# Kernel optimization log

Hardware: AMD Instinct MI355X
Metric: run time of the kernel (lower is better)

The kernel has to match this reference:

```python
import jax, jax.numpy as jnp
import numpy as np

B, K, D = 32768, 64, 64
GAIN = 1.0
LOG_2PI = float(np.log(2.0 * np.pi))


def setup_inputs() -> dict:
    key = jax.random.key(0)
    k1, k2, k3, k4 = jax.random.split(key, 4)
    return {
        "x": jax.random.normal(k1, (B, D), jnp.float32),
        "means_raw": jax.random.normal(k2, (K, D), jnp.float32),
        "scale_raw": jax.random.normal(k3, (K, D, D), jnp.float32),
        "weights_raw": jax.random.normal(k4, (K,), jnp.float32),
    }


def reference(x, means_raw, scale_raw, weights_raw):
    # EqualizedLR reparametrization: w_eff = w * gain / sqrt(fan_in)
    means = means_raw * (GAIN / np.sqrt(K * D))              # [K, D]
    pre = scale_raw * (GAIN / np.sqrt(K * D * D))            # [K, D, D]
    # ExpScaleTril (diag=False): strict lower triangle + exp(diagonal)
    dvec = jnp.exp(jnp.diagonal(pre, axis1=-2, axis2=-1))    # [K, D]
    L = jnp.tril(pre, -1) + dvec[..., :, None] * jnp.eye(D, dtype=pre.dtype)  # [K, D, D]
    # mixture logits -> log weights (EqualizedLR then softmax parametrization)
    logw = jax.nn.log_softmax(weights_raw * (GAIN / np.sqrt(K)), axis=-1)    # [K]

    # Precompute L^{-1} per component (K,D small), then whiten via one big GEMM.
    eye = jnp.broadcast_to(jnp.eye(D, dtype=L.dtype), L.shape)
    Linv = jax.scipy.linalg.solve_triangular(L, eye, lower=True)             # [K, D, D]

    diff = x[:, None, :] - means[None, :, :]                 # [B, K, D]
    z = jnp.einsum('kij,bkj->bki', Linv, diff)               # whitened residuals [B, K, D]
    maha = jnp.sum(z * z, axis=-1)                           # [B, K]
    half_log_det = jnp.sum(jnp.log(dvec), axis=-1)           # [K]
    comp_lp = -0.5 * (maha + D * LOG_2PI) - half_log_det     # [B, K]

    lp = jax.scipy.special.logsumexp(comp_lp + logw, axis=-1)  # [B]
    return -jnp.mean(lp)
```

## Files before the change

kernel.cpp:

```cpp
#include <hip/hip_runtime.h>

#define LOG_2PI 1.8378770664093453f

typedef __attribute__((ext_vector_type(8))) short  short8;
typedef __attribute__((ext_vector_type(4))) float  float4_;

__device__ __forceinline__ unsigned short f2bf(float f) {
  unsigned u = __builtin_bit_cast(unsigned, f);
  u += 0x7fffu + ((u >> 16) & 1u);
  return (unsigned short)(u >> 16);
}
__device__ __forceinline__ float bf2f(unsigned short h) {
  unsigned u = ((unsigned)h) << 16;
  return __builtin_bit_cast(float, u);
}
template <int CTRL>
__device__ __forceinline__ float dpp_add(float v) {
  int t = __builtin_amdgcn_mov_dpp(__builtin_bit_cast(int, v), CTRL, 0xf, 0xf, true);
  return v + __builtin_bit_cast(float, t);
}
__device__ __forceinline__ void async16(const void* g, void* l) {
  __builtin_amdgcn_global_load_lds((const __attribute__((address_space(1))) unsigned int*)g,
                                   (__attribute__((address_space(3))) unsigned int*)l, 16, 0, 0);
}

__global__ __launch_bounds__(256) void gmm_setup(
    const float* __restrict__ means_raw, const float* __restrict__ scale_raw,
    const float* __restrict__ weights_raw, unsigned short* __restrict__ Wf)
{
  const int k = blockIdx.x;
  const int t = threadIdx.x;
  const int lane = t & 63;
  const int wv = t >> 6;
  const int q = lane >> 4;
  const int jj = lane & 15;

  __shared__ float Plt[64][68];
  __shared__ float Vt[64][68];
  __shared__ __align__(16) unsigned short Vb[64][72];
  __shared__ float dg[64], rdg[64], mu_s[64], y_s[64];

  {
    const int i = t >> 2;
    const int c0 = (t & 3) * 16;
    float4_ v4[4];
    const float4_* src = (const float4_*)(scale_raw + (size_t)k * 4096 + i * 64 + c0);
    v4[0] = src[0]; v4[1] = src[1]; v4[2] = src[2]; v4[3] = src[3];
#pragma unroll
    for (int e = 0; e < 16; ++e) {
      const int c = c0 + e;
      const float val = ((const float*)v4)[e] * (1.0f / 512.0f);
      Plt[c][i] = (c < i) ? val : 0.0f;
      if (c == i) { dg[i] = val; rdg[i] = __expf(-val); }
    }
  }
  if (t < 64) mu_s[t] = means_raw[k * 64 + t] * (1.0f / 64.0f);
  __syncthreads();

  {
    const int j = wv * 16 + jj;
    float s[16];
#pragma unroll
    for (int i = 0; i < 16; ++i) s[i] = 0.0f;
#pragma unroll
    for (int m = 0; m < 64; ++m) {
      const float rm = rdg[m];
      float vcand = (m == j) ? rm : -s[m & 15] * rm;
      const float v = __shfl(vcand, (m >> 4) * 16 + jj, 64);
      if (q == (m >> 4)) {
        Vt[j][m] = v;
        Vb[j][m] = f2bf(v);
      }
      const float4_* prow = (const float4_*)&Plt[m][16 * q];
      const float4_ p0 = prow[0], p1 = prow[1], p2 = prow[2], p3 = prow[3];
      s[0]  += p0[0] * v; s[1]  += p0[1] * v; s[2]  += p0[2] * v; s[3]  += p0[3] * v;
      s[4]  += p1[0] * v; s[5]  += p1[1] * v; s[6]  += p1[2] * v; s[7]  += p1[3] * v;
      s[8]  += p2[0] * v; s[9]  += p2[1] * v; s[10] += p2[2] * v; s[11] += p2[3] * v;
      s[12] += p3[0] * v; s[13] += p3[1] * v; s[14] += p3[2] * v; s[15] += p3[3] * v;
    }
  }
  __syncthreads();

  {
    unsigned short* Wk = Wf + (size_t)k * 4608;
    const short8 a0 = *(const short8*)&Vb[16 * wv + jj][8 * q];
    const short8 a1 = *(const short8*)&Vb[16 * wv + jj][8 * q + 32];
#pragma unroll
    for (int t4 = 0; t4 < 4; ++t4) {
      const short8 b0 = *(const short8*)&Vb[jj + 16 * t4][8 * q];
      const short8 b1 = *(const short8*)&Vb[jj + 16 * t4][8 * q + 32];
      float4_ f = {0.f, 0.f, 0.f, 0.f};
      f = __builtin_amdgcn_mfma_f32_16x16x32_bf16(a0, b0, f, 0, 0, 0);
      f = __builtin_amdgcn_mfma_f32_16x16x32_bf16(a1, b1, f, 0, 0, 0);
#pragma unroll
      for (int r = 0; r < 4; ++r)
        Wk[(16 * wv + 4 * q + r) * 72 + jj + 16 * t4] = f2bf(-0.5f * f[r]);
    }
  }
  if (wv == 0) {
    float acc = 0.0f;
    for (int j2 = 0; j2 < 64; ++j2) acc += Vt[j2][lane] * mu_s[j2];
    y_s[lane] = acc;
  }
  __syncthreads();

  if (t < 64) {
    const int i = t;
    float ci = 0.0f;
#pragma unroll
    for (int m4 = 0; m4 < 16; ++m4) {
      const float4_ a4 = *(const float4_*)&Vt[i][4 * m4];
      const float4_ b4 = *(const float4_*)&y_s[4 * m4];
      ci += a4[0] * b4[0] + a4[1] * b4[1] + a4[2] * b4[2] + a4[3] * b4[3];
    }
    char* Wk = (char*)(Wf + (size_t)k * 4608);
    *(float*)(Wk + i * 144 + 128) = ci;
    float rq  = ci * mu_s[i];
    float dgv = dg[i];
    const float wr = weights_raw[i] * 0.125f;
    float mx = wr;
#pragma unroll
    for (int d = 1; d < 64; d <<= 1) mx = fmaxf(mx, __shfl_xor(mx, d, 64));
    float se = __expf(wr - mx);
#pragma unroll
    for (int d = 1; d < 64; d <<= 1) {
      se  += __shfl_xor(se, d, 64);
      rq  += __shfl_xor(rq, d, 64);
      dgv += __shfl_xor(dgv, d, 64);
    }
    if (i == 0) {
      const float wrk  = weights_raw[k] * 0.125f;
      const float logw = wrk - mx - __logf(se);
      *(float*)(Wk + 132) = -0.5f * rq - 32.0f * LOG_2PI - dgv + logw;
    }
  }
}

__global__ __launch_bounds__(256, 4) void gmm_main(
    const float* __restrict__ x, const unsigned short* __restrict__ Wf,
    unsigned short* __restrict__ ph)
{
  __shared__ __align__(16) unsigned short Wlds[2][2][4608];

  const int t = threadIdx.x;
  const int lane = t & 63;
  const int wv = t >> 6;
  const int q = lane >> 4;
  const int lr = lane & 15;
  const int kh = blockIdx.x & 3;
  const int rt = blockIdx.x >> 2;
  const int rowBase = rt * 128 + wv * 32;
  const int kbase = kh * 16;

  short8 a[2][2];
#pragma unroll
  for (int mt = 0; mt < 2; ++mt)
#pragma unroll
    for (int ks = 0; ks < 2; ++ks) {
      const float4_* xv = (const float4_*)(x + (size_t)(rowBase + mt * 16 + lr) * 64 + ks * 32 + q * 8);
      const float4_ lo = xv[0], hi = xv[1];
      short8 v;
      v[0] = f2bf(lo[0]); v[1] = f2bf(lo[1]); v[2] = f2bf(lo[2]); v[3] = f2bf(lo[3]);
      v[4] = f2bf(hi[0]); v[5] = f2bf(hi[1]); v[6] = f2bf(hi[2]); v[7] = f2bf(hi[3]);
      a[mt][ks] = v;
    }

  float xc[2][4][4];
#pragma unroll
  for (int mt = 0; mt < 2; ++mt)
#pragma unroll
    for (int r = 0; r < 4; ++r) {
      const float* xp = x + (size_t)(rowBase + mt * 16 + q * 4 + r) * 64 + lr;
#pragma unroll
      for (int t4 = 0; t4 < 4; ++t4) xc[mt][t4][r] = xp[16 * t4];
    }

  float sacc[2][4] = {{0, 0, 0, 0}, {0, 0, 0, 0}};

#define STAGE(g, slot)                                                          \
  {                                                                             \
    const unsigned short* src = Wf + (size_t)(kbase + 2 * (g)) * 4608 + t * 8;  \
    unsigned short* dst = &Wlds[slot][0][0] + t * 8;                            \
    async16(src,         dst);                                                  \
    async16(src + 2048,  dst + 2048);                                           \
    async16(src + 4096,  dst + 4096);                                           \
    async16(src + 6144,  dst + 6144);                                           \
    if (t < 128) async16(src + 8192, dst + 8192);                               \
  }

  STAGE(0, 0)
  __syncthreads();

  for (int g = 0; g < 8; ++g) {
    const int cur = g & 1;
    if (g < 7) STAGE(g + 1, cur ^ 1)
#pragma unroll
    for (int kk = 0; kk < 2; ++kk) {
      const unsigned short* wb = &Wlds[cur][kk][0];
      float cc[4];
#pragma unroll
      for (int t4 = 0; t4 < 4; ++t4)
        cc[t4] = *(const float*)(wb + (lr + 16 * t4) * 72 + 64);
      const float bk = *(const float*)(wb + 66) + 90.0f;

      short8 b[2][4];
#pragma unroll
      for (int t4 = 0; t4 < 4; ++t4)
#pragma unroll
        for (int ks = 0; ks < 2; ++ks)
          b[ks][t4] = *(const short8*)(wb + (lr + 16 * t4) * 72 + 8 * q + 32 * ks);

      float4_ f[2][4];
#pragma unroll
      for (int mt = 0; mt < 2; ++mt)
#pragma unroll
        for (int t4 = 0; t4 < 4; ++t4) {
          const float cv = cc[t4];
          float4_ acc = {cv, cv, cv, cv};
          acc = __builtin_amdgcn_mfma_f32_16x16x32_bf16(a[mt][0], b[0][t4], acc, 0, 0, 0);
          acc = __builtin_amdgcn_mfma_f32_16x16x32_bf16(a[mt][1], b[1][t4], acc, 0, 0, 0);
          f[mt][t4] = acc;
        }

#pragma unroll
      for (int mt = 0; mt < 2; ++mt)
#pragma unroll
        for (int r = 0; r < 4; ++r) {
          float sdot = xc[mt][0][r] * f[mt][0][r] + xc[mt][1][r] * f[mt][1][r]
                     + xc[mt][2][r] * f[mt][2][r] + xc[mt][3][r] * f[mt][3][r];
          sdot = dpp_add<0x121>(sdot);
          sdot = dpp_add<0x122>(sdot);
          sdot = dpp_add<0x124>(sdot);
          sdot = dpp_add<0x128>(sdot);
          sacc[mt][r] += __expf(sdot + bk);
        }
    }
    __syncthreads();
  }
#undef STAGE

  if (lr == 0) {
#pragma unroll
    for (int mt = 0; mt < 2; ++mt)
#pragma unroll
      for (int r = 0; r < 4; ++r)
        ph[(size_t)kh * 32768 + rowBase + mt * 16 + q * 4 + r] = f2bf(sacc[mt][r]);
  }
}

__global__ __launch_bounds__(256) void gmm_final1(const unsigned short* __restrict__ ph,
                                                  float* __restrict__ p1)
{
  const int t = threadIdx.x;
  const int r0 = blockIdx.x * 512 + t;
  float v = 0.0f;
#pragma unroll
  for (int h = 0; h < 2; ++h) {
    const int row = r0 + 256 * h;
    const float s = bf2f(ph[row]) + bf2f(ph[32768 + row])
                  + bf2f(ph[65536 + row]) + bf2f(ph[98304 + row]);
    v += __logf(s) - 90.0f;
  }
#pragma unroll
  for (int d = 1; d < 64; d <<= 1) v += __shfl_xor(v, d, 64);
  __shared__ float s4[4];
  if ((t & 63) == 0) s4[t >> 6] = v;
  __syncthreads();
  if (t == 0) p1[blockIdx.x] = s4[0] + s4[1] + s4[2] + s4[3];
}

__global__ __launch_bounds__(64) void gmm_final2(const float* __restrict__ p1,
                                                 float* __restrict__ out)
{
  float v = p1[threadIdx.x];
#pragma unroll
  for (int d = 1; d < 64; d <<= 1) v += __shfl_xor(v, d, 64);
  if (threadIdx.x == 0) out[0] = -v * (1.0f / 32768.0f);
}

extern "C" void kernel_launch(void* const* d_in, const int* in_sizes, int n_in,
                              void* d_out, int out_size, void* d_ws, size_t ws_size,
                              hipStream_t stream)
{
  const float* x           = (const float*)d_in[0];
  const float* means_raw   = (const float*)d_in[1];
  const float* scale_raw   = (const float*)d_in[2];
  const float* weights_raw = (const float*)d_in[3];
  float* out = (float*)d_out;

  char* ws = (char*)d_ws;
  unsigned short* Wf = (unsigned short*)ws;
  unsigned short* ph = (unsigned short*)(ws + 589824);
  float* p1          = (float*)(ws + 851968);

  gmm_setup<<<64, 256, 0, stream>>>(means_raw, scale_raw, weights_raw, Wf);
  gmm_main<<<1024, 256, 0, stream>>>(x, Wf, ph);
  gmm_final1<<<64, 256, 0, stream>>>(ph, p1);
  gmm_final2<<<1, 64, 0, stream>>>(p1, out);
}
```

Before: 109.4 us.

## Fuse final reductions into main kernel via atomics and last-block finish

Removes the two final reduction kernels. The main kernel now atomically adds per-row partial sums into an fp32 buffer, and the last block to finish (tracked by an atomic counter) computes the log-mean itself. The grid is doubled, so each block handles 8 components instead of 16, which raises parallelism. The log2e scaling is folded into the setup weights so the inner loop can use exp2. The changes trade two launches for atomic traffic and a serial tail reduction run by a single block.

```diff
diff --git a/kernel.cpp b/kernel.cpp
--- a/kernel.cpp
+++ b/kernel.cpp
@@ -1,6 +1,7 @@
 #include <hip/hip_runtime.h>
 
 #define LOG_2PI 1.8378770664093453f
+#define LOG2E   1.4426950408889634f
 
 typedef __attribute__((ext_vector_type(8))) short  short8;
 typedef __attribute__((ext_vector_type(4))) float  float4_;
@@ -10,10 +11,6 @@
   u += 0x7fffu + ((u >> 16) & 1u);
   return (unsigned short)(u >> 16);
 }
-__device__ __forceinline__ float bf2f(unsigned short h) {
-  unsigned u = ((unsigned)h) << 16;
-  return __builtin_bit_cast(float, u);
-}
 template <int CTRL>
 __device__ __forceinline__ float dpp_add(float v) {
   int t = __builtin_amdgcn_mov_dpp(__builtin_bit_cast(int, v), CTRL, 0xf, 0xf, true);
@@ -26,7 +23,8 @@
 
 __global__ __launch_bounds__(256) void gmm_setup(
     const float* __restrict__ means_raw, const float* __restrict__ scale_raw,
-    const float* __restrict__ weights_raw, unsigned short* __restrict__ Wf)
+    const float* __restrict__ weights_raw, unsigned short* __restrict__ Wf,
+    float* __restrict__ ph, unsigned int* __restrict__ done)
 {
   const int k = blockIdx.x;
   const int t = threadIdx.x;
@@ -34,6 +32,10 @@
   const int wv = t >> 6;
   const int q = lane >> 4;
   const int jj = lane & 15;
+
+  ph[k * 512 + t] = 0.0f;
+  ph[k * 512 + 256 + t] = 0.0f;
+  if (k == 0 && t == 0) *done = 0u;
 
   __shared__ float Plt[64][68];
   __shared__ float Vt[64][68];
@@ -94,7 +96,7 @@
       f = __builtin_amdgcn_mfma_f32_16x16x32_bf16(a1, b1, f, 0, 0, 0);
 #pragma unroll
       for (int r = 0; r < 4; ++r)
-        Wk[(16 * wv + 4 * q + r) * 72 + jj + 16 * t4] = f2bf(-0.5f * f[r]);
+        Wk[(16 * wv + 4 * q + r) * 72 + jj + 16 * t4] = f2bf(-0.5f * LOG2E * f[r]);
     }
   }
   if (wv == 0) {
@@ -114,7 +116,7 @@
       ci += a4[0] * b4[0] + a4[1] * b4[1] + a4[2] * b4[2] + a4[3] * b4[3];
     }
     char* Wk = (char*)(Wf + (size_t)k * 4608);
-    *(float*)(Wk + i * 144 + 128) = ci;
+    *(float*)(Wk + i * 144 + 128) = LOG2E * ci;
     float rq  = ci * mu_s[i];
     float dgv = dg[i];
     const float wr = weights_raw[i] * 0.125f;
@@ -131,14 +133,16 @@
     if (i == 0) {
       const float wrk  = weights_raw[k] * 0.125f;
       const float logw = wrk - mx - __logf(se);
-      *(float*)(Wk + 132) = -0.5f * rq - 32.0f * LOG_2PI - dgv + logw;
+      const float beta = -0.5f * rq - 32.0f * LOG_2PI - dgv + logw;
+      *(float*)(Wk + 132) = LOG2E * (beta + 90.0f);
     }
   }
 }
 
 __global__ __launch_bounds__(256, 4) void gmm_main(
     const float* __restrict__ x, const unsigned short* __restrict__ Wf,
-    unsigned short* __restrict__ ph)
+    float* __restrict__ ph, unsigned int* __restrict__ done,
+    float* __restrict__ out)
 {
   __shared__ __align__(16) unsigned short Wlds[2][2][4608];
 
@@ -147,10 +151,10 @@
   const int wv = t >> 6;
   const int q = lane >> 4;
   const int lr = lane & 15;
-  const int kh = blockIdx.x & 3;
-  const int rt = blockIdx.x >> 2;
+  const int kh = blockIdx.x & 7;
+  const int rt = blockIdx.x >> 3;
   const int rowBase = rt * 128 + wv * 32;
-  const int kbase = kh * 16;
+  const int kbase = kh * 8;
 
   short8 a[2][2];
 #pragma unroll
@@ -191,9 +195,9 @@
   STAGE(0, 0)
   __syncthreads();
 
-  for (int g = 0; g < 8; ++g) {
+  for (int g = 0; g < 4; ++g) {
     const int cur = g & 1;
-    if (g < 7) STAGE(g + 1, cur ^ 1)
+    if (g < 3) STAGE(g + 1, cur ^ 1)
 #pragma unroll
     for (int kk = 0; kk < 2; ++kk) {
       const unsigned short* wb = &Wlds[cur][kk][0];
@@ -201,7 +205,7 @@
 #pragma unroll
       for (int t4 = 0; t4 < 4; ++t4)
         cc[t4] = *(const float*)(wb + (lr + 16 * t4) * 72 + 64);
-      const float bk = *(const float*)(wb + 66) + 90.0f;
+      const float bk = *(const float*)(wb + 66);
 
       short8 b[2][4];
 #pragma unroll
@@ -232,7 +236,7 @@
           sdot = dpp_add<0x122>(sdot);
           sdot = dpp_add<0x124>(sdot);
           sdot = dpp_add<0x128>(sdot);
-          sacc[mt][r] += __expf(sdot + bk);
+          sacc[mt][r] += exp2f(sdot + bk);
         }
     }
     __syncthreads();
@@ -244,38 +248,26 @@
     for (int mt = 0; mt < 2; ++mt)
 #pragma unroll
       for (int r = 0; r < 4; ++r)
-        ph[(size_t)kh * 32768 + rowBase + mt * 16 + q * 4 + r] = f2bf(sacc[mt][r]);
-  }
-}
-
-__global__ __launch_bounds__(256) void gmm_final1(const unsigned short* __restrict__ ph,
-                                                  float* __restrict__ p1)
-{
-  const int t = threadIdx.x;
-  const int r0 = blockIdx.x * 512 + t;
-  float v = 0.0f;
-#pragma unroll
-  for (int h = 0; h < 2; ++h) {
-    const int row = r0 + 256 * h;
-    const float s = bf2f(ph[row]) + bf2f(ph[32768 + row])
-                  + bf2f(ph[65536 + row]) + bf2f(ph[98304 + row]);
-    v += __logf(s) - 90.0f;
-  }
-#pragma unroll
-  for (int d = 1; d < 64; d <<= 1) v += __shfl_xor(v, d, 64);
-  __shared__ float s4[4];
-  if ((t & 63) == 0) s4[t >> 6] = v;
-  __syncthreads();
-  if (t == 0) p1[blockIdx.x] = s4[0] + s4[1] + s4[2] + s4[3];
-}
-
-__global__ __launch_bounds__(64) void gmm_final2(const float* __restrict__ p1,
-                                                 float* __restrict__ out)
-{
-  float v = p1[threadIdx.x];
-#pragma unroll
-  for (int d = 1; d < 64; d <<= 1) v += __shfl_xor(v, d, 64);
-  if (threadIdx.x == 0) out[0] = -v * (1.0f / 32768.0f);
+        atomicAdd(&ph[rowBase + mt * 16 + q * 4 + r], sacc[mt][r]);
+  }
+
+  __threadfence();
+  __shared__ int lastFlag;
+  if (t == 0) lastFlag = (atomicAdd(done, 1u) == 2047u) ? 1 : 0;
+  __syncthreads();
+  if (lastFlag) {
+    float v = 0.0f;
+    for (int i = t; i < 32768; i += 256) {
+      const float s = __hip_atomic_load(&ph[i], __ATOMIC_RELAXED, __HIP_MEMORY_SCOPE_AGENT);
+      v += __logf(s) - 90.0f;
+    }
+#pragma unroll
+    for (int d = 1; d < 64; d <<= 1) v += __shfl_xor(v, d, 64);
+    __shared__ float s4[4];
+    if ((t & 63) == 0) s4[t >> 6] = v;
+    __syncthreads();
+    if (t == 0) out[0] = -(s4[0] + s4[1] + s4[2] + s4[3]) * (1.0f / 32768.0f);
+  }
 }
 
 extern "C" void kernel_launch(void* const* d_in, const int* in_sizes, int n_in,
@@ -290,11 +282,9 @@
 
   char* ws = (char*)d_ws;
   unsigned short* Wf = (unsigned short*)ws;
-  unsigned short* ph = (unsigned short*)(ws + 589824);
-  float* p1          = (float*)(ws + 851968);
-
-  gmm_setup<<<64, 256, 0, stream>>>(means_raw, scale_raw, weights_raw, Wf);
-  gmm_main<<<1024, 256, 0, stream>>>(x, Wf, ph);
-  gmm_final1<<<64, 256, 0, stream>>>(ph, p1);
-  gmm_final2<<<1, 64, 0, stream>>>(p1, out);
-}
+  float* ph          = (float*)(ws + 589824);
+  unsigned int* done = (unsigned int*)(ws + 720896);
+
+  gmm_setup<<<64, 256, 0, stream>>>(means_raw, scale_raw, weights_raw, Wf, ph, done);
+  gmm_main<<<2048, 256, 0, stream>>>(x, Wf, ph, done, out);
+}
```

New measurement: 348.8 us. 3.19x slower.
